# Optimization experiments

Measured on AMD Instinct MI355X. Metric: run time of the kernel, lower is better.

## Reference

```python
import jax, jax.numpy as jnp
import numpy as np
import math

H = 80; W = 80
FOVX = math.pi / 2.0; FOVY = math.pi / 2.0
TANX = math.tan(FOVX * 0.5); TANY = math.tan(FOVY * 0.5)
FOCAL_X = W / (2.0 * TANX); FOCAL_Y = H / (2.0 * TANY)
SCALE_MOD = 1.0
N_GAUSS = 4096; K_GEOM = 1024; K_SH = 1024

SH_C0 = 0.28209479177387814
SH_C1 = 0.4886025119029199
C2 = [1.0925484305920792, -1.0925484305920792, 0.31539156525252005, -1.0925484305920792, 0.5462742152960396]
C3 = [-0.5900435899266435, 2.890611442640554, -0.4570457994644658, 0.3731763325901154, -0.4570457994644658, 1.445305721320277, -0.5900435899266435]


def eval_sh3(sh, d):
    # sh: [N,16,3], d: [N,3] unit view directions -> clamped RGB [N,3]
    x, y, z = d[:, 0:1], d[:, 1:2], d[:, 2:3]
    xx, yy, zz = x * x, y * y, z * z
    xy, yz, xz = x * y, y * z, x * z
    res = (SH_C0 * sh[:, 0]
           - SH_C1 * y * sh[:, 1] + SH_C1 * z * sh[:, 2] - SH_C1 * x * sh[:, 3]
           + C2[0] * xy * sh[:, 4] + C2[1] * yz * sh[:, 5]
           + C2[2] * (2.0 * zz - xx - yy) * sh[:, 6]
           + C2[3] * xz * sh[:, 7] + C2[4] * (xx - yy) * sh[:, 8]
           + C3[0] * y * (3.0 * xx - yy) * sh[:, 9] + C3[1] * xy * z * sh[:, 10]
           + C3[2] * y * (4.0 * zz - xx - yy) * sh[:, 11]
           + C3[3] * z * (2.0 * zz - 3.0 * xx - 3.0 * yy) * sh[:, 12]
           + C3[4] * x * (4.0 * zz - xx - yy) * sh[:, 13]
           + C3[5] * z * (xx - yy) * sh[:, 14]
           + C3[6] * x * (xx - yy - 3.0 * zz) * sh[:, 15])
    return jnp.maximum(res + 0.5, 0.0)


def quat_to_rotmat(q):
    # q: [N,4] normalized (w,x,y,z) -> [N,3,3]
    w, x, y, z = q[:, 0], q[:, 1], q[:, 2], q[:, 3]
    r0 = jnp.stack([1 - 2 * (y * y + z * z), 2 * (x * y - w * z), 2 * (x * z + w * y)], -1)
    r1 = jnp.stack([2 * (x * y + w * z), 1 - 2 * (x * x + z * z), 2 * (y * z - w * x)], -1)
    r2 = jnp.stack([2 * (x * z - w * y), 2 * (y * z + w * x), 1 - 2 * (x * x + y * y)], -1)
    return jnp.stack([r0, r1, r2], axis=1)


def _forward(means3D, sh, sh_indices, g_indices, opacities, scales, scale_factors, rotations, extrinsic, bg):
    N = means3D.shape[0]
    # row-vector convention as in the torch wrapper: p_hom = [x,y,z,1] @ view
    R3 = extrinsic[:3, :3]; t3 = extrinsic[3, :3]
    p_view = means3D @ R3 + t3  # [N,3] camera space
    tx, ty, tz = p_view[:, 0], p_view[:, 1], p_view[:, 2]
    in_front = tz > 0.2  # near-plane cull as in CUDA kernel
    tz_s = jnp.where(in_front, tz, 1.0)
    # NDC (projection matrix reduces to x/(z tanx), y/(z tany)) then ndc2Pix
    gx = ((tx / (tz_s * TANX) + 1.0) * W - 1.0) * 0.5
    gy = ((ty / (tz_s * TANY) + 1.0) * H - 1.0) * 0.5
    # indexed 3D covariance: Sigma = R diag(s^2) R^T, codebook gathers
    s = scales[g_indices] * scale_factors * SCALE_MOD  # [N,3]
    q = rotations[g_indices]
    q = q / jnp.linalg.norm(q, axis=1, keepdims=True)
    Rm = quat_to_rotmat(q)
    cov3D = jnp.einsum('nij,nj,nkj->nik', Rm, s * s, Rm)
    # EWA splat: world->cam rotation is R3^T under row-vector storage
    Wm = R3.T
    cov_cam = jnp.einsum('ij,njk,lk->nil', Wm, cov3D, Wm)
    limx = 1.3 * TANX; limy = 1.3 * TANY
    txc = jnp.clip(tx / tz_s, -limx, limx) * tz_s
    tyc = jnp.clip(ty / tz_s, -limy, limy) * tz_s
    J = jnp.zeros((N, 2, 3), means3D.dtype)
    J = J.at[:, 0, 0].set(FOCAL_X / tz_s).at[:, 0, 2].set(-FOCAL_X * txc / (tz_s * tz_s))
    J = J.at[:, 1, 1].set(FOCAL_Y / tz_s).at[:, 1, 2].set(-FOCAL_Y * tyc / (tz_s * tz_s))
    cov2d = jnp.einsum('nij,njk,nlk->nil', J, cov_cam, J)
    a = cov2d[:, 0, 0] + 0.3; b = cov2d[:, 0, 1]; c = cov2d[:, 1, 1] + 0.3
    det = a * c - b * b
    valid = in_front & (det > 0)
    det_s = jnp.where(det != 0, det, 1.0)
    ca = c / det_s; cb = -b / det_s; cc = a / det_s  # conic
    mid = 0.5 * (a + c)
    lam1 = mid + jnp.sqrt(jnp.maximum(0.1, mid * mid - det))
    radii = jnp.where(valid, jnp.ceil(3.0 * jnp.sqrt(lam1)), 0.0).astype(jnp.int32)
    # SH -> RGB, view dir from camera position (extrinsic.inverse()[3,:3])
    campos = jnp.linalg.inv(extrinsic)[3, :3]
    dirs = means3D - campos
    dirs = dirs / jnp.linalg.norm(dirs, axis=1, keepdims=True)
    color = eval_sh3(sh[sh_indices], dirs)  # [N,3]
    # global front-to-back depth sort
    depth = jnp.where(valid, tz, jnp.inf)
    order = jnp.argsort(depth)
    gx_s, gy_s = gx[order], gy[order]
    ca_s, cb_s, cc_s = ca[order], cb[order], cc[order]
    op_s = opacities[order, 0]; col_s = color[order]; val_s = valid[order]
    # pixel grid (pixel centers at integer coords as in renderCUDA)
    ys, xs = jnp.meshgrid(jnp.arange(H, dtype=means3D.dtype), jnp.arange(W, dtype=means3D.dtype), indexing='ij')
    px = xs.reshape(-1); py = ys.reshape(-1)  # [P]
    dx = gx_s[None, :] - px[:, None]  # [P,N]
    dy = gy_s[None, :] - py[:, None]
    power = -0.5 * (ca_s * dx * dx + cc_s * dy * dy) - cb_s * dx * dy
    alpha = jnp.minimum(0.99, op_s[None, :] * jnp.exp(jnp.minimum(power, 0.0)))
    keep = (power <= 0.0) & val_s[None, :] & (alpha >= 1.0 / 255.0)
    alpha = jnp.where(keep, alpha, 0.0)
    om = 1.0 - alpha
    T_inc = jnp.cumprod(om, axis=1)
    inc = T_inc >= 1e-4  # early-termination prefix (T monotone)
    T_excl = jnp.concatenate([jnp.ones((px.shape[0], 1), om.dtype), T_inc[:, :-1]], axis=1)
    w = alpha * T_excl * inc
    T_final = jnp.prod(jnp.where(inc, om, 1.0), axis=1)
    out = w @ col_s + T_final[:, None] * bg[None, :]  # [P,3]
    color_img = jnp.transpose(out.reshape(H, W, 3), (2, 0, 1))  # [3,H,W]
    return color_img, radii


def setup_inputs() -> dict:
    key = jax.random.key(0)
    ks = jax.random.split(key, 9)
    xy = (jax.random.uniform(ks[0], (N_GAUSS, 2)) - 0.5) * 4.0
    z = jax.random.uniform(ks[1], (N_GAUSS, 1)) * 4.0 + 2.0
    means3D = jnp.concatenate([xy, z], axis=1)  # inside the view frustum
    sh = jax.random.normal(ks[2], (K_SH, 16, 3)) * 0.3
    sh_indices = jax.random.randint(ks[3], (N_GAUSS,), 0, K_SH)
    g_indices = jax.random.randint(ks[4], (N_GAUSS,), 0, K_GEOM)
    opacities = jax.random.uniform(ks[5], (N_GAUSS, 1), minval=0.1, maxval=0.99)
    scales = jax.random.uniform(ks[6], (K_GEOM, 3), minval=0.01, maxval=0.08)
    scale_factors = jax.random.uniform(ks[7], (N_GAUSS, 1), minval=0.5, maxval=1.5)
    rotations = jax.random.normal(ks[8], (K_GEOM, 4))
    extrinsic = jnp.eye(4, dtype=jnp.float32)
    bg = jnp.zeros((3,), jnp.float32)
    return dict(means3D=means3D, sh=sh, sh_indices=sh_indices, g_indices=g_indices,
                opacities=opacities, scales=scales, scale_factors=scale_factors,
                rotations=rotations, extrinsic=extrinsic, bg=bg)


def reference(means3D, sh, sh_indices, g_indices, opacities, scales, scale_factors, rotations, extrinsic, bg):
    return _forward(means3D, sh, sh_indices, g_indices, opacities, scales, scale_factors, rotations, extrinsic, bg)
```

## Files before the change

### kernel.cpp

```cpp
#include <hip/hip_runtime.h>
#include <math.h>

#define NG 4096
#define WI 80
#define HI 80
#define NPIX (WI*HI)
#define FOCAL 40.0f
#define LIM 1.3f
#define NPART 4
#define RANGE (NG/NPART)

#define SH_C0 0.28209479177387814f
#define SH_C1 0.4886025119029199f

#define U0_OFF 0
#define U1_OFF (64*1024)
#define U2_OFF (128*1024)
#define S0_OFF (192*1024)
#define B1_OFF (256*1024)
#define B2_OFF (320*1024)
#define B3_OFF (384*1024)
#define KD_OFF (400*1024)
#define RK_OFF (432*1024)
#define PP_OFF (448*1024)

__device__ inline float rdlane(float v, int l) {
  return __uint_as_float(__builtin_amdgcn_readlane(__float_as_uint(v), l));
}

__global__ __launch_bounds__(256) void prep_k(
    const float* __restrict__ means, const float* __restrict__ sh,
    const int* __restrict__ shidx, const int* __restrict__ gidx,
    const float* __restrict__ opac, const float* __restrict__ scales,
    const float* __restrict__ sfac, const float* __restrict__ rots,
    const float* __restrict__ ext, char* __restrict__ wsb,
    float* __restrict__ radii_out)
{
  int i = blockIdx.x*blockDim.x + threadIdx.x;
  if (i >= NG) return;
  float e0=ext[0],  e1=ext[1],  e2=ext[2];
  float e4=ext[4],  e5=ext[5],  e6=ext[6];
  float e8=ext[8],  e9=ext[9],  e10=ext[10];
  float e12=ext[12], e13=ext[13], e14=ext[14];
  float m0=means[3*i+0], m1=means[3*i+1], m2=means[3*i+2];
  float tx = m0*e0 + m1*e4 + m2*e8  + e12;
  float ty = m0*e1 + m1*e5 + m2*e9  + e13;
  float tz = m0*e2 + m1*e6 + m2*e10 + e14;
  bool infront = tz > 0.2f;
  float tzs = infront ? tz : 1.0f;
  float inv_tzs = 1.0f / tzs;
  float gx = ((tx*inv_tzs + 1.0f)*WI - 1.0f)*0.5f;
  float gy = ((ty*inv_tzs + 1.0f)*HI - 1.0f)*0.5f;

  int gi = gidx[i];
  float sf = sfac[i];
  float s0 = scales[3*gi+0]*sf, s1 = scales[3*gi+1]*sf, s2 = scales[3*gi+2]*sf;
  float qw = rots[4*gi+0], qx = rots[4*gi+1], qy = rots[4*gi+2], qz = rots[4*gi+3];
  float qinv = rsqrtf(qw*qw+qx*qx+qy*qy+qz*qz);
  qw*=qinv; qx*=qinv; qy*=qinv; qz*=qinv;
  float r00 = 1.0f - 2.0f*(qy*qy+qz*qz);
  float r01 = 2.0f*(qx*qy - qw*qz);
  float r02 = 2.0f*(qx*qz + qw*qy);
  float r10 = 2.0f*(qx*qy + qw*qz);
  float r11 = 1.0f - 2.0f*(qx*qx+qz*qz);
  float r12 = 2.0f*(qy*qz - qw*qx);
  float r20 = 2.0f*(qx*qz - qw*qy);
  float r21 = 2.0f*(qy*qz + qw*qx);
  float r22 = 1.0f - 2.0f*(qx*qx+qy*qy);
  float v0 = s0*s0, v1 = s1*s1, v2 = s2*s2;
  float C00 = r00*r00*v0 + r01*r01*v1 + r02*r02*v2;
  float C01 = r00*r10*v0 + r01*r11*v1 + r02*r12*v2;
  float C02 = r00*r20*v0 + r01*r21*v1 + r02*r22*v2;
  float C11 = r10*r10*v0 + r11*r11*v1 + r12*r12*v2;
  float C12 = r10*r20*v0 + r11*r21*v1 + r12*r22*v2;
  float C22 = r20*r20*v0 + r21*r21*v1 + r22*r22*v2;
  float W0x=e0, W0y=e4, W0z=e8;
  float W1x=e1, W1y=e5, W1z=e9;
  float W2x=e2, W2y=e6, W2z=e10;
  float B00 = W0x*C00 + W0y*C01 + W0z*C02;
  float B01 = W0x*C01 + W0y*C11 + W0z*C12;
  float B02 = W0x*C02 + W0y*C12 + W0z*C22;
  float B10 = W1x*C00 + W1y*C01 + W1z*C02;
  float B11 = W1x*C01 + W1y*C11 + W1z*C12;
  float B12 = W1x*C02 + W1y*C12 + W1z*C22;
  float B20 = W2x*C00 + W2y*C01 + W2z*C02;
  float B21 = W2x*C01 + W2y*C11 + W2z*C12;
  float B22 = W2x*C02 + W2y*C12 + W2z*C22;
  float V00 = B00*W0x + B01*W0y + B02*W0z;
  float V02 = B00*W2x + B01*W2y + B02*W2z;
  float V01 = B00*W1x + B01*W1y + B02*W1z;
  float V11 = B10*W1x + B11*W1y + B12*W1z;
  float V12 = B10*W2x + B11*W2y + B12*W2z;
  float V22 = B20*W2x + B21*W2y + B22*W2z;
  float txz = tx*inv_tzs, tyz = ty*inv_tzs;
  float txc = fminf(fmaxf(txz, -LIM), LIM) * tzs;
  float tyc = fminf(fmaxf(tyz, -LIM), LIM) * tzs;
  float jx  = FOCAL*inv_tzs;
  float jy  = FOCAL*inv_tzs;
  float jz0 = -FOCAL*txc*inv_tzs*inv_tzs;
  float jz1 = -FOCAL*tyc*inv_tzs*inv_tzs;
  float c00 = jx*jx*V00 + 2.0f*jx*jz0*V02 + jz0*jz0*V22;
  float c01 = jx*jy*V01 + jx*jz1*V02 + jz0*jy*V12 + jz0*jz1*V22;
  float c11 = jy*jy*V11 + 2.0f*jy*jz1*V12 + jz1*jz1*V22;
  float a = c00 + 0.3f;
  float b = c01;
  float cf = c11 + 0.3f;
  float det = a*cf - b*b;
  bool valid = infront && (det > 0.0f);
  float dets = (det != 0.0f) ? det : 1.0f;
  float ca = cf/dets, cb = -b/dets, cc = a/dets;
  float mid = 0.5f*(a+cf);
  float lam1 = mid + sqrtf(fmaxf(0.1f, mid*mid - det));
  float radf = valid ? ceilf(3.0f*sqrtf(lam1)) : 0.0f;
  radii_out[i] = radf;

  float op = valid ? opac[i] : 0.0f;
  float L2 = 2.0f*fmaxf(0.0f, logf(255.0f*op));
  float rcx = valid ? sqrtf(L2*a)  + 0.01f : 0.0f;
  float rcy = valid ? sqrtf(L2*cf) + 0.01f : 0.0f;

  float cp0 = -(e12*e0 + e13*e1 + e14*e2);
  float cp1 = -(e12*e4 + e13*e5 + e14*e6);
  float cp2 = -(e12*e8 + e13*e9 + e14*e10);
  float dx0 = m0-cp0, dy0 = m1-cp1, dz0 = m2-cp2;
  float dn = rsqrtf(dx0*dx0+dy0*dy0+dz0*dz0);
  float x = dx0*dn, y = dy0*dn, z = dz0*dn;
  float xx=x*x, yy=y*y, zz=z*z;
  float xy=x*y, yz=y*z, xz=x*z;
  float bf[16];
  bf[0]  = SH_C0;
  bf[1]  = -SH_C1*y;
  bf[2]  =  SH_C1*z;
  bf[3]  = -SH_C1*x;
  bf[4]  =  1.0925484305920792f*xy;
  bf[5]  = -1.0925484305920792f*yz;
  bf[6]  =  0.31539156525252005f*(2.0f*zz-xx-yy);
  bf[7]  = -1.0925484305920792f*xz;
  bf[8]  =  0.5462742152960396f*(xx-yy);
  bf[9]  = -0.5900435899266435f*y*(3.0f*xx-yy);
  bf[10] =  2.890611442640554f*xy*z;
  bf[11] = -0.4570457994644658f*y*(4.0f*zz-xx-yy);
  bf[12] =  0.3731763325901154f*z*(2.0f*zz-3.0f*xx-3.0f*yy);
  bf[13] = -0.4570457994644658f*x*(4.0f*zz-xx-yy);
  bf[14] =  1.445305721320277f*z*(xx-yy);
  bf[15] = -0.5900435899266435f*x*(xx-yy-3.0f*zz);
  const float* S = sh + (long)shidx[i]*48;
  float cr=0.f, cg=0.f, cbl=0.f;
  #pragma unroll
  for (int j=0;j<16;j++) {
    float w = bf[j];
    cr  += w*S[j*3+0];
    cg  += w*S[j*3+1];
    cbl += w*S[j*3+2];
  }
  cr  = fmaxf(cr +0.5f, 0.0f);
  cg  = fmaxf(cg +0.5f, 0.0f);
  cbl = fmaxf(cbl+0.5f, 0.0f);

  float depth = infront ? tz : __builtin_inff();
  ((float4*)(wsb + U0_OFF))[i] = make_float4(gx, gy, rcx, rcy);
  ((float4*)(wsb + U1_OFF))[i] = make_float4(ca, cb, cc, op);
  ((float4*)(wsb + U2_OFF))[i] = make_float4(cr, cg, cbl, 0.0f);
  ((unsigned long long*)(wsb + KD_OFF))[i] =
      ((unsigned long long)__float_as_uint(depth) << 32) | (unsigned)i;
  ((int*)(wsb + RK_OFF))[i] = 0;
}

__global__ __launch_bounds__(256) void rank_k(const char* __restrict__ wsb,
                                              int* __restrict__ rank)
{
  const unsigned long long* kd = (const unsigned long long*)(wsb + KD_OFF);
  int tid = threadIdx.x;
  int i = blockIdx.x*256 + tid;
  unsigned long long ki = kd[i];
  int jb = blockIdx.y*256;
  int r = 0;
  #pragma unroll 8
  for (int jj = 0; jj < 256; ++jj) {
    unsigned long long kj = kd[jb + ((tid + jj) & 255)];
    r += (kj < ki);
  }
  atomicAdd(&rank[i], r);
}

__global__ __launch_bounds__(256) void scatter_k(char* __restrict__ wsb)
{
  int i = blockIdx.x*256 + threadIdx.x;
  int r = ((const int*)(wsb + RK_OFF))[i];
  float4 u0 = ((const float4*)(wsb + U0_OFF))[i];
  float4 u1 = ((const float4*)(wsb + U1_OFF))[i];
  float4 u2 = ((const float4*)(wsb + U2_OFF))[i];
  ((float4*)(wsb + S0_OFF))[r] = u0;
  ((float4*)(wsb + B1_OFF))[r] = make_float4(u0.x, u0.y, u1.x, u1.y);
  ((float4*)(wsb + B2_OFF))[r] = make_float4(u1.z, u1.w, u2.x, u2.y);
  ((float*) (wsb + B3_OFF))[r] = u2.z;
}

__global__ __launch_bounds__(512) void tile_k(const char* __restrict__ wsb,
                                              float4* __restrict__ pp)
{
  __shared__ float4 sb1[RANGE];
  __shared__ float4 sb2[RANGE];
  __shared__ float  sb3[RANGE];
  __shared__ int    wcnt[2][8];
  __shared__ float  pT[8][64], pR[8][64], pG[8][64], pB[8][64];
  const float4* S0 = (const float4*)(wsb + S0_OFF);
  const float4* B1 = (const float4*)(wsb + B1_OFF);
  const float4* B2 = (const float4*)(wsb + B2_OFF);
  const float*  B3 = (const float*) (wsb + B3_OFF);

  int tid = threadIdx.x;
  int wv = tid >> 6, lane = tid & 63;
  int part = blockIdx.x / 100;
  int tile = blockIdx.x % 100;
  int base = part * RANGE;
  int x0 = (tile % 10) * 8, y0 = (tile / 10) * 8;
  float bx0 = (float)x0, bx1 = (float)(x0+7);
  float by0 = (float)y0, by1 = (float)(y0+7);

  int scnt = 0;
  #pragma unroll
  for (int c = 0; c < RANGE/512; ++c) {
    int i = base + c*512 + tid;
    float4 v = S0[i];
    bool hit = (v.z > 0.0f) &&
               (v.x + v.z >= bx0) && (v.x - v.z <= bx1) &&
               (v.y + v.w >= by0) && (v.y - v.w <= by1);
    unsigned long long m = __ballot(hit);
    int par = c & 1;
    if (lane == 0) wcnt[par][wv] = __popcll(m);
    __syncthreads();
    int pre = 0, tot = 0;
    #pragma unroll
    for (int w = 0; w < 8; ++w) {
      int cw = wcnt[par][w];
      pre += (w < wv) ? cw : 0;
      tot += cw;
    }
    if (hit) {
      int pos = scnt + pre + __popcll(m & ((1ull<<lane)-1ull));
      sb1[pos] = B1[i];
      sb2[pos] = B2[i];
      sb3[pos] = B3[i];
    }
    scnt += tot;
  }
  __syncthreads();
  int cnt = scnt;

  float px = (float)(x0 + (lane & 7));
  float py = (float)(y0 + (lane >> 3));
  int seg = (cnt + 7) >> 3;
  int s0i = wv*seg;
  int s1i = s0i + seg; if (s1i > cnt) s1i = cnt;
  float T = 1.0f, ar = 0.f, ag = 0.f, ab = 0.f;
  for (int eb = s0i; eb < s1i; eb += 64) {
    int nn = s1i - eb; if (nn > 64) nn = 64;
    float4 q1 = (lane < nn) ? sb1[eb+lane] : make_float4(0.f,0.f,0.f,0.f);
    float4 q2 = (lane < nn) ? sb2[eb+lane] : make_float4(0.f,0.f,0.f,0.f);
    float  r3 = (lane < nn) ? sb3[eb+lane] : 0.f;
    for (int c16 = 0; c16 < nn && __ballot(T >= 1e-4f); c16 += 16) {
      int ce = c16 + 16; if (ce > nn) ce = nn;
      for (int e = c16; e < ce; ++e) {
        float gxe = rdlane(q1.x, e), gye = rdlane(q1.y, e);
        float cae = rdlane(q1.z, e), cbe = rdlane(q1.w, e);
        float cce = rdlane(q2.x, e), ope = rdlane(q2.y, e);
        float cre = rdlane(q2.z, e), cge = rdlane(q2.w, e);
        float cble = rdlane(r3, e);
        float dx = gxe - px, dy = gye - py;
        float power = -0.5f*(cae*dx*dx + cce*dy*dy) - cbe*dx*dy;
        float al = 0.0f;
        if (power <= 0.0f) {
          float av = fminf(0.99f, ope*__expf(power));
          if (av >= (1.0f/255.0f)) al = av;
        }
        float w = al*T;
        ar += w*cre; ag += w*cge; ab += w*cble;
        T *= 1.0f - al;
      }
    }
  }
  pT[wv][lane]=T; pR[wv][lane]=ar; pG[wv][lane]=ag; pB[wv][lane]=ab;
  __syncthreads();

  if (tid < 64) {
    float Tg = 1.0f, r = 0.f, g2 = 0.f, b2 = 0.f;
    #pragma unroll
    for (int w = 0; w < 8; ++w) {
      r  += Tg*pR[w][tid];
      g2 += Tg*pG[w][tid];
      b2 += Tg*pB[w][tid];
      Tg *= pT[w][tid];
    }
    int p = (y0 + (tid>>3))*WI + (x0 + (tid&7));
    pp[part*NPIX + p] = make_float4(Tg, r, g2, b2);
  }
}

__global__ __launch_bounds__(256) void combine_k(const float4* __restrict__ pp,
                                                 const float* __restrict__ bg,
                                                 float* __restrict__ out)
{
  int p = blockIdx.x*256 + threadIdx.x;
  float T = 1.0f, r = 0.f, g = 0.f, b = 0.f;
  #pragma unroll
  for (int part = 0; part < NPART; ++part) {
    float4 q = pp[part*NPIX + p];
    r += T*q.y; g += T*q.z; b += T*q.w;
    T *= q.x;
  }
  out[0*NPIX+p] = r + T*bg[0];
  out[1*NPIX+p] = g + T*bg[1];
  out[2*NPIX+p] = b + T*bg[2];
}

extern "C" void kernel_launch(void* const* d_in, const int* in_sizes, int n_in,
                              void* d_out, int out_size, void* d_ws, size_t ws_size,
                              hipStream_t stream) {
  const float* means  = (const float*)d_in[0];
  const float* sh     = (const float*)d_in[1];
  const int*   shidx  = (const int*)  d_in[2];
  const int*   gidx   = (const int*)  d_in[3];
  const float* opac   = (const float*)d_in[4];
  const float* scales = (const float*)d_in[5];
  const float* sfac   = (const float*)d_in[6];
  const float* rots   = (const float*)d_in[7];
  const float* ext    = (const float*)d_in[8];
  const float* bg     = (const float*)d_in[9];
  float* out = (float*)d_out;
  char* wsb = (char*)d_ws;
  float4* pp = (float4*)(wsb + PP_OFF);

  prep_k<<<NG/256, 256, 0, stream>>>(means, sh, shidx, gidx, opac, scales, sfac,
                                     rots, ext, wsb, out + 3*NPIX);
  dim3 rg(NG/256, NG/256);
  rank_k<<<rg, 256, 0, stream>>>(wsb, (int*)(wsb + RK_OFF));
  scatter_k<<<NG/256, 256, 0, stream>>>(wsb);
  tile_k<<<100*NPART, 512, 0, stream>>>(wsb, pp);
  combine_k<<<NPIX/256, 256, 0, stream>>>(pp, bg, out);
}
```

Before: 95.17 us.

## Fuse rank with scatter and fold combine into tile kernel via tickets

Result: slower. 262.5 us (+175.8%).

```diff
diff --git a/kernel.cpp b/kernel.cpp
--- a/kernel.cpp
+++ b/kernel.cpp
@@ -21,14 +21,16 @@
 #define B2_OFF (320*1024)
 #define B3_OFF (384*1024)
 #define KD_OFF (400*1024)
-#define RK_OFF (432*1024)
 #define PP_OFF (448*1024)
+#define TK_OFF (852*1024)
+
+typedef unsigned long long u64;
 
 __device__ inline float rdlane(float v, int l) {
   return __uint_as_float(__builtin_amdgcn_readlane(__float_as_uint(v), l));
 }
 
-__global__ __launch_bounds__(256) void prep_k(
+__global__ __launch_bounds__(64) void prep_k(
     const float* __restrict__ means, const float* __restrict__ sh,
     const int* __restrict__ shidx, const int* __restrict__ gidx,
     const float* __restrict__ opac, const float* __restrict__ scales,
@@ -37,6 +39,7 @@
     float* __restrict__ radii_out)
 {
   int i = blockIdx.x*blockDim.x + threadIdx.x;
+  if (i < 100) ((int*)(wsb + TK_OFF))[i] = 0;
   if (i >= NG) return;
   float e0=ext[0],  e1=ext[1],  e2=ext[2];
   float e4=ext[4],  e5=ext[5],  e6=ext[6];
@@ -161,53 +164,55 @@
   ((float4*)(wsb + U0_OFF))[i] = make_float4(gx, gy, rcx, rcy);
   ((float4*)(wsb + U1_OFF))[i] = make_float4(ca, cb, cc, op);
   ((float4*)(wsb + U2_OFF))[i] = make_float4(cr, cg, cbl, 0.0f);
-  ((unsigned long long*)(wsb + KD_OFF))[i] =
-      ((unsigned long long)__float_as_uint(depth) << 32) | (unsigned)i;
-  ((int*)(wsb + RK_OFF))[i] = 0;
-}
-
-__global__ __launch_bounds__(256) void rank_k(const char* __restrict__ wsb,
-                                              int* __restrict__ rank)
+  ((u64*)(wsb + KD_OFF))[i] =
+      ((u64)__float_as_uint(depth) << 32) | (unsigned)i;
+}
+
+__global__ __launch_bounds__(1024) void rankscatter_k(char* __restrict__ wsb)
 {
-  const unsigned long long* kd = (const unsigned long long*)(wsb + KD_OFF);
-  int tid = threadIdx.x;
-  int i = blockIdx.x*256 + tid;
-  unsigned long long ki = kd[i];
-  int jb = blockIdx.y*256;
+  __shared__ int partial[256][4];
+  const u64* kd = (const u64*)(wsb + KD_OFF);
+  int t = threadIdx.x;
+  int il = t & 255, q = t >> 8;
+  int i = blockIdx.x*256 + il;
+  u64 ki = kd[i];
+  int jb = q*1024;
   int r = 0;
   #pragma unroll 8
-  for (int jj = 0; jj < 256; ++jj) {
-    unsigned long long kj = kd[jb + ((tid + jj) & 255)];
+  for (int jj = 0; jj < 1024; ++jj) {
+    u64 kj = kd[jb + ((il + jj) & 1023)];
     r += (kj < ki);
   }
-  atomicAdd(&rank[i], r);
-}
-
-__global__ __launch_bounds__(256) void scatter_k(char* __restrict__ wsb)
-{
-  int i = blockIdx.x*256 + threadIdx.x;
-  int r = ((const int*)(wsb + RK_OFF))[i];
-  float4 u0 = ((const float4*)(wsb + U0_OFF))[i];
-  float4 u1 = ((const float4*)(wsb + U1_OFF))[i];
-  float4 u2 = ((const float4*)(wsb + U2_OFF))[i];
-  ((float4*)(wsb + S0_OFF))[r] = u0;
-  ((float4*)(wsb + B1_OFF))[r] = make_float4(u0.x, u0.y, u1.x, u1.y);
-  ((float4*)(wsb + B2_OFF))[r] = make_float4(u1.z, u1.w, u2.x, u2.y);
-  ((float*) (wsb + B3_OFF))[r] = u2.z;
-}
-
-__global__ __launch_bounds__(512) void tile_k(const char* __restrict__ wsb,
-                                              float4* __restrict__ pp)
+  partial[il][q] = r;
+  __syncthreads();
+  if (q == 0) {
+    int rr = partial[il][0] + partial[il][1] + partial[il][2] + partial[il][3];
+    float4 u0 = ((const float4*)(wsb + U0_OFF))[i];
+    float4 u1 = ((const float4*)(wsb + U1_OFF))[i];
+    float4 u2 = ((const float4*)(wsb + U2_OFF))[i];
+    ((float4*)(wsb + S0_OFF))[rr] = u0;
+    ((float4*)(wsb + B1_OFF))[rr] = make_float4(u0.x, u0.y, u1.x, u1.y);
+    ((float4*)(wsb + B2_OFF))[rr] = make_float4(u1.z, u1.w, u2.x, u2.y);
+    ((float*) (wsb + B3_OFF))[rr] = u2.z;
+  }
+}
+
+__global__ __launch_bounds__(512) void tile_k(char* __restrict__ wsb,
+                                              const float* __restrict__ bg,
+                                              float* __restrict__ out)
 {
   __shared__ float4 sb1[RANGE];
   __shared__ float4 sb2[RANGE];
   __shared__ float  sb3[RANGE];
   __shared__ int    wcnt[2][8];
   __shared__ float  pT[8][64], pR[8][64], pG[8][64], pB[8][64];
+  __shared__ int    sticket;
   const float4* S0 = (const float4*)(wsb + S0_OFF);
   const float4* B1 = (const float4*)(wsb + B1_OFF);
   const float4* B2 = (const float4*)(wsb + B2_OFF);
   const float*  B3 = (const float*) (wsb + B3_OFF);
+  float4* pp = (float4*)(wsb + PP_OFF);
+  int* ticket = (int*)(wsb + TK_OFF);
 
   int tid = threadIdx.x;
   int wv = tid >> 6, lane = tid & 63;
@@ -283,6 +288,7 @@
   pT[wv][lane]=T; pR[wv][lane]=ar; pG[wv][lane]=ag; pB[wv][lane]=ab;
   __syncthreads();
 
+  int p = (y0 + (tid>>3))*WI + (x0 + (tid&7));
   if (tid < 64) {
     float Tg = 1.0f, r = 0.f, g2 = 0.f, b2 = 0.f;
     #pragma unroll
@@ -292,26 +298,27 @@
       b2 += Tg*pB[w][tid];
       Tg *= pT[w][tid];
     }
-    int p = (y0 + (tid>>3))*WI + (x0 + (tid&7));
     pp[part*NPIX + p] = make_float4(Tg, r, g2, b2);
   }
-}
-
-__global__ __launch_bounds__(256) void combine_k(const float4* __restrict__ pp,
-                                                 const float* __restrict__ bg,
-                                                 float* __restrict__ out)
-{
-  int p = blockIdx.x*256 + threadIdx.x;
-  float T = 1.0f, r = 0.f, g = 0.f, b = 0.f;
-  #pragma unroll
-  for (int part = 0; part < NPART; ++part) {
-    float4 q = pp[part*NPIX + p];
-    r += T*q.y; g += T*q.z; b += T*q.w;
-    T *= q.x;
-  }
-  out[0*NPIX+p] = r + T*bg[0];
-  out[1*NPIX+p] = g + T*bg[1];
-  out[2*NPIX+p] = b + T*bg[2];
+  __threadfence();
+  __syncthreads();
+  if (tid == 0) sticket = atomicAdd(&ticket[tile], 1);
+  __syncthreads();
+  if (sticket == NPART-1) {
+    __threadfence();
+    if (tid < 64) {
+      float T2 = 1.0f, r = 0.f, g = 0.f, b = 0.f;
+      #pragma unroll
+      for (int pt = 0; pt < NPART; ++pt) {
+        float4 qq = pp[pt*NPIX + p];
+        r += T2*qq.y; g += T2*qq.z; b += T2*qq.w;
+        T2 *= qq.x;
+      }
+      out[0*NPIX+p] = r + T2*bg[0];
+      out[1*NPIX+p] = g + T2*bg[1];
+      out[2*NPIX+p] = b + T2*bg[2];
+    }
+  }
 }
 
 extern "C" void kernel_launch(void* const* d_in, const int* in_sizes, int n_in,
@@ -329,13 +336,9 @@
   const float* bg     = (const float*)d_in[9];
   float* out = (float*)d_out;
   char* wsb = (char*)d_ws;
-  float4* pp = (float4*)(wsb + PP_OFF);
-
-  prep_k<<<NG/256, 256, 0, stream>>>(means, sh, shidx, gidx, opac, scales, sfac,
-                                     rots, ext, wsb, out + 3*NPIX);
-  dim3 rg(NG/256, NG/256);
-  rank_k<<<rg, 256, 0, stream>>>(wsb, (int*)(wsb + RK_OFF));
-  scatter_k<<<NG/256, 256, 0, stream>>>(wsb);
-  tile_k<<<100*NPART, 512, 0, stream>>>(wsb, pp);
-  combine_k<<<NPIX/256, 256, 0, stream>>>(pp, bg, out);
-}
+
+  prep_k<<<NG/64, 64, 0, stream>>>(means, sh, shidx, gidx, opac, scales, sfac,
+                                   rots, ext, wsb, out + 3*NPIX);
+  rankscatter_k<<<NG/256, 1024, 0, stream>>>(wsb);
+  tile_k<<<100*NPART, 512, 0, stream>>>(wsb, bg, out);
+}
```
